# Kernel tuning notes

Hardware: AMD Instinct MI355X
Metric: run time of the kernel (lower is better)

The kernel has to match this reference:

```python
import jax, jax.numpy as jnp
import numpy as np

N_NODES = 100000
N_EDGES = 3200000
IN_F, HID, OUT = 3, 32, 1
NEG_SLOPE = 0.2


def _glorot(key, shape):
    fan_in, fan_out = shape[0], shape[-1]
    lim = jnp.sqrt(6.0 / (fan_in + fan_out)).astype(jnp.float32)
    return jax.random.uniform(key, shape, jnp.float32, -lim, lim)


def setup_inputs() -> dict:
    key = jax.random.key(0)
    ks = jax.random.split(key, 12)
    x = jax.random.normal(ks[0], (N_NODES, IN_F), jnp.float32)
    edge_index = jax.random.randint(ks[1], (2, N_EDGES), 0, N_NODES, jnp.int32)
    return {
        "x": x,
        "edge_index": edge_index,
        "W1": _glorot(ks[2], (IN_F, HID)),
        "att_src1": _glorot(ks[3], (1, HID))[0],
        "att_dst1": _glorot(ks[4], (1, HID))[0],
        "b1": jnp.zeros((HID,), jnp.float32),
        "W2": _glorot(ks[5], (HID, HID)),
        "att_src2": _glorot(ks[6], (1, HID))[0],
        "att_dst2": _glorot(ks[7], (1, HID))[0],
        "b2": jnp.zeros((HID,), jnp.float32),
        "Wl": _glorot(ks[8], (HID, OUT)),
        "bl": jnp.zeros((OUT,), jnp.float32),
    }


def gat_layer(x, src, dst, W, att_src, att_dst, b):
    # h: [N, HID] dense transform
    h = x @ W
    # per-node attention halves (compute once per node, gather per edge)
    a_s = h @ att_src  # [N]
    a_d = h @ att_dst  # [N]
    logits = jax.nn.leaky_relu(a_s[src] + a_d[dst], NEG_SLOPE)  # [E+N]
    # segment-softmax over incoming edges of each dst node
    m = jax.ops.segment_max(logits, dst, num_segments=N_NODES)
    m = jnp.where(jnp.isfinite(m), m, 0.0)
    ex = jnp.exp(logits - m[dst])
    denom = jax.ops.segment_sum(ex, dst, num_segments=N_NODES)
    coef = ex / (denom[dst] + 1e-16)
    # weighted scatter-aggregate of source messages
    out = jax.ops.segment_sum(coef[:, None] * h[src], dst, num_segments=N_NODES)
    return out + b


def reference(x, edge_index, W1, att_src1, att_dst1, b1, W2, att_src2, att_dst2, b2, Wl, bl):
    # PyG GATConv default: add self-loops
    loops = jnp.arange(N_NODES, dtype=edge_index.dtype)
    src = jnp.concatenate([edge_index[0], loops])
    dst = jnp.concatenate([edge_index[1], loops])
    h = gat_layer(x, src, dst, W1, att_src1, att_dst1, b1)
    h = jax.nn.relu(h)  # dropout is identity in eval
    h = gat_layer(h, src, dst, W2, att_src2, att_dst2, b2)
    h = jax.nn.relu(h)
    return h @ Wl + bl
```

## Files before the change

kernel.cpp:

```cpp
#include <hip/hip_runtime.h>
#include <hip/hip_fp16.h>

#define HID 32
#define BN 132
#define NBPAD 1024
#define BSTRIDE 5120
#define CHUNK 8192

__device__ __forceinline__ float lrelu(float x) { return x > 0.0f ? x : 0.2f * x; }

__global__ void k_transform1(const float* __restrict__ x,
                             const float* __restrict__ W1,
                             const float* __restrict__ att_src,
                             const float* __restrict__ att_dst,
                             __half* __restrict__ hh,
                             float* __restrict__ a_s,
                             float* __restrict__ a_d,
                             int* __restrict__ cursor,
                             int N)
{
    int tid = blockIdx.x * blockDim.x + threadIdx.x;
    if (tid < NBPAD) cursor[tid] = 0;
    int n = tid >> 5;
    int f = tid & 31;
    if (n >= N) return;
    float x0 = x[n * 3 + 0], x1 = x[n * 3 + 1], x2 = x[n * 3 + 2];
    float hv = x0 * W1[f] + x1 * W1[HID + f] + x2 * W1[2 * HID + f];
    hh[(size_t)n * HID + f] = __float2half(hv);
    float as = hv * att_src[f];
    float ad = hv * att_dst[f];
    #pragma unroll
    for (int m = 16; m >= 1; m >>= 1) {
        as += __shfl_xor(as, m, 32);
        ad += __shfl_xor(ad, m, 32);
    }
    if (f == 0) { a_s[n] = as; a_d[n] = ad; }
}

__global__ void __launch_bounds__(256) k_binscatter(const int* __restrict__ src,
                                                    const int* __restrict__ dst,
                                                    int* __restrict__ cursor,
                                                    unsigned int* __restrict__ packed,
                                                    int NB, int E)
{
    __shared__ int stage[CHUNK];
    __shared__ int lhist[NBPAD], lexcl[NBPAD], lbase[NBPAD], lcur[NBPAD];
    __shared__ int arr[256];
    int t = threadIdx.x;
    for (int i = t; i < NBPAD; i += 256) { lhist[i] = 0; lcur[i] = 0; }
    __syncthreads();
    int base = blockIdx.x * CHUNK;
    int cnt = E - base; if (cnt > CHUNK) cnt = CHUNK;
    for (int i = t; i < cnt; i += 256)
        atomicAdd(&lhist[dst[base + i] / BN], 1);
    __syncthreads();
    int b0 = 4 * t;
    int c0 = lhist[b0], c1 = lhist[b0 + 1], c2 = lhist[b0 + 2], c3 = lhist[b0 + 3];
    int s = c0 + c1 + c2 + c3;
    arr[t] = s;
    __syncthreads();
    for (int o = 1; o < 256; o <<= 1) {
        int v = (t >= o) ? arr[t - o] : 0;
        __syncthreads();
        arr[t] += v;
        __syncthreads();
    }
    int ex = arr[t] - s;
    lexcl[b0] = ex; lexcl[b0 + 1] = ex + c0;
    lexcl[b0 + 2] = ex + c0 + c1; lexcl[b0 + 3] = ex + c0 + c1 + c2;
    for (int b = t; b < NB; b += 256)
        if (lhist[b]) lbase[b] = b * BSTRIDE + atomicAdd(&cursor[b], lhist[b]);
    __syncthreads();
    for (int i = t; i < cnt; i += 256) {
        int d = dst[base + i];
        int sv = src[base + i];
        int b = d / BN;
        int dl = d - b * BN;
        int idx = lexcl[b] + atomicAdd(&lcur[b], 1);
        stage[idx] = (int)((unsigned)sv | ((unsigned)dl << 17));
    }
    __syncthreads();
    for (int i = t; i < cnt; i += 256) {
        int lo = 0, hi = NB - 1;
        while (lo < hi) {
            int mid = (lo + hi + 1) >> 1;
            if (lexcl[mid] <= i) lo = mid; else hi = mid - 1;
        }
        int gpos = lbase[lo] + (i - lexcl[lo]);
        if (gpos < (lo + 1) * BSTRIDE)
            packed[gpos] = (unsigned)stage[i];
    }
}

__global__ void __launch_bounds__(256) k_bucket_csr(unsigned int* __restrict__ packed,
                                                    const int* __restrict__ cursor,
                                                    int* __restrict__ offsets,
                                                    int* __restrict__ deg, int N)
{
    __shared__ int lcsr[BSTRIDE];
    __shared__ int lhist[256], lscan[256], lcur[256];
    int b = blockIdx.x, t = threadIdx.x;
    int base = b * BSTRIDE;
    int cnt = cursor[b]; if (cnt > BSTRIDE) cnt = BSTRIDE;
    lhist[t] = 0; lcur[t] = 0;
    __syncthreads();
    for (int i = t; i < cnt; i += 256)
        atomicAdd(&lhist[(packed[base + i] >> 17) & 255], 1);
    __syncthreads();
    lscan[t] = lhist[t];
    __syncthreads();
    for (int o = 1; o < 256; o <<= 1) {
        int v = (t >= o) ? lscan[t - o] : 0;
        __syncthreads();
        lscan[t] += v;
        __syncthreads();
    }
    int node = b * BN + t;
    int excl = lscan[t] - lhist[t];
    if (t < BN && node < N) { offsets[node] = base + excl; deg[node] = lhist[t]; }
    for (int i = t; i < cnt; i += 256) {
        unsigned int p = packed[base + i];
        int dl = (p >> 17) & 255;
        int pos = atomicAdd(&lcur[dl], 1);
        lcsr[(lscan[dl] - lhist[dl]) + pos] = (int)(p & 0x1FFFF);
    }
    __syncthreads();
    for (int i = t; i < cnt; i += 256)
        packed[base + i] = (unsigned)lcsr[i];
}

__device__ __forceinline__ void agg_core(const __half* __restrict__ hh,
                                         const float* __restrict__ a_s,
                                         float a_dn, float a_sn,
                                         const float* __restrict__ b,
                                         int n, int f, int off, int dg,
                                         const int* __restrict__ csr_src,
                                         float& vx, float& vy)
{
    float ex = __expf(lrelu(a_sn + a_dn));
    float den = ex;
    float2 hs = __half22float2(*(const __half2*)(hh + (size_t)n * HID + 2 * f));
    float accx = ex * hs.x;
    float accy = ex * hs.y;
    for (int base = 0; base < dg; base += 16) {
        int m = dg - base; if (m > 16) m = 16;
        int sv = 0;
        float exv = 0.0f;
        if (f < m) {
            sv = csr_src[off + base + f];
            exv = __expf(lrelu(a_s[sv] + a_dn));
        }
        int j = 0;
        for (; j + 8 <= m; j += 8) {
            int s0 = __shfl(sv, j, 16), s1 = __shfl(sv, j + 1, 16);
            int s2 = __shfl(sv, j + 2, 16), s3 = __shfl(sv, j + 3, 16);
            int s4 = __shfl(sv, j + 4, 16), s5 = __shfl(sv, j + 5, 16);
            int s6 = __shfl(sv, j + 6, 16), s7 = __shfl(sv, j + 7, 16);
            float e0 = __shfl(exv, j, 16), e1 = __shfl(exv, j + 1, 16);
            float e2 = __shfl(exv, j + 2, 16), e3 = __shfl(exv, j + 3, 16);
            float e4 = __shfl(exv, j + 4, 16), e5 = __shfl(exv, j + 5, 16);
            float e6 = __shfl(exv, j + 6, 16), e7 = __shfl(exv, j + 7, 16);
            __half2 p0 = *(const __half2*)(hh + (size_t)s0 * HID + 2 * f);
            __half2 p1 = *(const __half2*)(hh + (size_t)s1 * HID + 2 * f);
            __half2 p2 = *(const __half2*)(hh + (size_t)s2 * HID + 2 * f);
            __half2 p3 = *(const __half2*)(hh + (size_t)s3 * HID + 2 * f);
            __half2 p4 = *(const __half2*)(hh + (size_t)s4 * HID + 2 * f);
            __half2 p5 = *(const __half2*)(hh + (size_t)s5 * HID + 2 * f);
            __half2 p6 = *(const __half2*)(hh + (size_t)s6 * HID + 2 * f);
            __half2 p7 = *(const __half2*)(hh + (size_t)s7 * HID + 2 * f);
            float2 q0 = __half22float2(p0), q1 = __half22float2(p1);
            float2 q2 = __half22float2(p2), q3 = __half22float2(p3);
            float2 q4 = __half22float2(p4), q5 = __half22float2(p5);
            float2 q6 = __half22float2(p6), q7 = __half22float2(p7);
            den += ((e0 + e1) + (e2 + e3)) + ((e4 + e5) + (e6 + e7));
            accx = fmaf(e0, q0.x, accx); accy = fmaf(e0, q0.y, accy);
            accx = fmaf(e1, q1.x, accx); accy = fmaf(e1, q1.y, accy);
            accx = fmaf(e2, q2.x, accx); accy = fmaf(e2, q2.y, accy);
            accx = fmaf(e3, q3.x, accx); accy = fmaf(e3, q3.y, accy);
            accx = fmaf(e4, q4.x, accx); accy = fmaf(e4, q4.y, accy);
            accx = fmaf(e5, q5.x, accx); accy = fmaf(e5, q5.y, accy);
            accx = fmaf(e6, q6.x, accx); accy = fmaf(e6, q6.y, accy);
            accx = fmaf(e7, q7.x, accx); accy = fmaf(e7, q7.y, accy);
        }
        for (; j + 4 <= m; j += 4) {
            int s0 = __shfl(sv, j, 16), s1 = __shfl(sv, j + 1, 16);
            int s2 = __shfl(sv, j + 2, 16), s3 = __shfl(sv, j + 3, 16);
            float e0 = __shfl(exv, j, 16), e1 = __shfl(exv, j + 1, 16);
            float e2 = __shfl(exv, j + 2, 16), e3 = __shfl(exv, j + 3, 16);
            __half2 p0 = *(const __half2*)(hh + (size_t)s0 * HID + 2 * f);
            __half2 p1 = *(const __half2*)(hh + (size_t)s1 * HID + 2 * f);
            __half2 p2 = *(const __half2*)(hh + (size_t)s2 * HID + 2 * f);
            __half2 p3 = *(const __half2*)(hh + (size_t)s3 * HID + 2 * f);
            float2 q0 = __half22float2(p0), q1 = __half22float2(p1);
            float2 q2 = __half22float2(p2), q3 = __half22float2(p3);
            den += (e0 + e1) + (e2 + e3);
            accx = fmaf(e0, q0.x, accx); accy = fmaf(e0, q0.y, accy);
            accx = fmaf(e1, q1.x, accx); accy = fmaf(e1, q1.y, accy);
            accx = fmaf(e2, q2.x, accx); accy = fmaf(e2, q2.y, accy);
            accx = fmaf(e3, q3.x, accx); accy = fmaf(e3, q3.y, accy);
        }
        for (; j < m; ++j) {
            int s0 = __shfl(sv, j, 16);
            float e0 = __shfl(exv, j, 16);
            float2 q0 = __half22float2(*(const __half2*)(hh + (size_t)s0 * HID + 2 * f));
            den += e0;
            accx = fmaf(e0, q0.x, accx);
            accy = fmaf(e0, q0.y, accy);
        }
    }
    float inv = 1.0f / (den + 1e-16f);
    vx = fmaxf(accx * inv + b[2 * f], 0.0f);
    vy = fmaxf(accy * inv + b[2 * f + 1], 0.0f);
}

__global__ void __launch_bounds__(256) k_agg_mid(const __half* __restrict__ hh,
                          const float* __restrict__ a_s,
                          const float* __restrict__ a_d,
                          const int* __restrict__ offsets,
                          const int* __restrict__ deg,
                          const int* __restrict__ csr_src,
                          const float* __restrict__ b,
                          const float* __restrict__ W2,
                          const float* __restrict__ att_src2,
                          const float* __restrict__ att_dst2,
                          __half* __restrict__ hh_out,
                          float* __restrict__ a_s_out,
                          float* __restrict__ a_d_out,
                          int N)
{
    int tid = blockIdx.x * blockDim.x + threadIdx.x;
    int n = tid >> 4;
    int f = tid & 15;
    if (n >= N) return;
    float vx, vy;
    agg_core(hh, a_s, a_d[n], a_s[n], b, n, f, offsets[n], deg[n], csr_src, vx, vy);
    float hx = 0.0f, hy = 0.0f;
    #pragma unroll
    for (int k = 0; k < 16; ++k) {
        float va = __shfl(vx, k, 16);
        float vb = __shfl(vy, k, 16);
        float2 w0 = *(const float2*)(W2 + (2 * k) * HID + 2 * f);
        float2 w1 = *(const float2*)(W2 + (2 * k + 1) * HID + 2 * f);
        hx = fmaf(va, w0.x, hx); hy = fmaf(va, w0.y, hy);
        hx = fmaf(vb, w1.x, hx); hy = fmaf(vb, w1.y, hy);
    }
    *(__half2*)(hh_out + (size_t)n * HID + 2 * f) = __floats2half2_rn(hx, hy);
    float as = hx * att_src2[2 * f] + hy * att_src2[2 * f + 1];
    float ad = hx * att_dst2[2 * f] + hy * att_dst2[2 * f + 1];
    #pragma unroll
    for (int m2 = 8; m2 >= 1; m2 >>= 1) {
        as += __shfl_xor(as, m2, 16);
        ad += __shfl_xor(ad, m2, 16);
    }
    if (f == 0) { a_s_out[n] = as; a_d_out[n] = ad; }
}

__global__ void __launch_bounds__(256) k_agg_out(const __half* __restrict__ hh,
                          const float* __restrict__ a_s,
                          const float* __restrict__ a_d,
                          const int* __restrict__ offsets,
                          const int* __restrict__ deg,
                          const int* __restrict__ csr_src,
                          const float* __restrict__ b,
                          const float* __restrict__ Wl,
                          const float* __restrict__ bl,
                          float* __restrict__ out,
                          int N)
{
    int tid = blockIdx.x * blockDim.x + threadIdx.x;
    int n = tid >> 4;
    int f = tid & 15;
    if (n >= N) return;
    float vx, vy;
    agg_core(hh, a_s, a_d[n], a_s[n], b, n, f, offsets[n], deg[n], csr_src, vx, vy);
    float y = vx * Wl[2 * f] + vy * Wl[2 * f + 1];
    #pragma unroll
    for (int m2 = 8; m2 >= 1; m2 >>= 1) {
        y += __shfl_xor(y, m2, 16);
    }
    if (f == 0) out[n] = y + bl[0];
}

extern "C" void kernel_launch(void* const* d_in, const int* in_sizes, int n_in,
                              void* d_out, int out_size, void* d_ws, size_t ws_size,
                              hipStream_t stream)
{
    const float* x        = (const float*)d_in[0];
    const int*   eidx     = (const int*)d_in[1];
    const float* W1       = (const float*)d_in[2];
    const float* att_src1 = (const float*)d_in[3];
    const float* att_dst1 = (const float*)d_in[4];
    const float* b1       = (const float*)d_in[5];
    const float* W2       = (const float*)d_in[6];
    const float* att_src2 = (const float*)d_in[7];
    const float* att_dst2 = (const float*)d_in[8];
    const float* b2       = (const float*)d_in[9];
    const float* Wl       = (const float*)d_in[10];
    const float* bl       = (const float*)d_in[11];
    float* out = (float*)d_out;

    int N = in_sizes[0] / 3;
    int E = in_sizes[1] / 2;
    const int* src = eidx;
    const int* dst = eidx + E;
    int NB = (N + BN - 1) / BN;

    size_t szNHh = (size_t)N * HID * 2;
    size_t szN4  = (size_t)N * 4;
    size_t szPK  = (size_t)NB * BSTRIDE * 4;

    char* ws = (char*)d_ws;
    __half* h1h    = (__half*)ws; ws += szNHh;
    __half* h2h    = (__half*)ws; ws += szNHh;
    unsigned int* packed = (unsigned int*)ws; ws += szPK;
    float*  a_s1   = (float*)ws;  ws += szN4;
    float*  a_d1   = (float*)ws;  ws += szN4;
    float*  a_s2   = (float*)ws;  ws += szN4;
    float*  a_d2   = (float*)ws;  ws += szN4;
    int*    deg    = (int*)ws;    ws += szN4;
    int*    offsets= (int*)ws;    ws += szN4;
    int*    cursor = (int*)ws;    ws += NBPAD * 4;

    const int B = 256;
    int gridNode32 = (N * HID + B - 1) / B;
    int gridNode16 = (N * 16 + B - 1) / B;
    int gridBin    = (E + CHUNK - 1) / CHUNK;

    k_transform1<<<gridNode32, B, 0, stream>>>(x, W1, att_src1, att_dst1,
                                               h1h, a_s1, a_d1, cursor, N);
    k_binscatter<<<gridBin, B, 0, stream>>>(src, dst, cursor, packed, NB, E);
    k_bucket_csr<<<NB, B, 0, stream>>>(packed, cursor, offsets, deg, N);
    k_agg_mid<<<gridNode16, B, 0, stream>>>(h1h, a_s1, a_d1, offsets, deg, (const int*)packed,
                                            b1, W2, att_src2, att_dst2,
                                            h2h, a_s2, a_d2, N);
    k_agg_out<<<gridNode16, B, 0, stream>>>(h2h, a_s2, a_d2, offsets, deg, (const int*)packed,
                                            b2, Wl, bl, out, N);
}
```

Before: 272.4 us.

## Fuse bucket CSR build into aggregation kernels and replace binary search with bin-id table

Removes the separate bucket-to-CSR kernel. Each aggregation kernel now rebuilds the per-bucket CSR in shared memory and aggregates that bucket's nodes with 512-thread blocks, one block per bucket. Binscatter drops its per-element binary search for a shared-memory table of bin ids, and CHUNK and NBPAD shrink to 4096 and 768. The intent is to cut one kernel launch and the global CSR round trip, and to avoid keeping offsets and degrees in global memory. In exchange the CSR is built twice and aggregation parallelism drops to about 758 blocks with uneven per-node work.

New measurement: 259.7 us. -4.7%, faster.

```diff
diff --git a/kernel.cpp b/kernel.cpp
--- a/kernel.cpp
+++ b/kernel.cpp
@@ -3,9 +3,9 @@
 
 #define HID 32
 #define BN 132
-#define NBPAD 1024
+#define NBPAD 768
 #define BSTRIDE 5120
-#define CHUNK 8192
+#define CHUNK 4096
 
 __device__ __forceinline__ float lrelu(float x) { return x > 0.0f ? x : 0.2f * x; }
 
@@ -41,9 +41,10 @@
                                                     const int* __restrict__ dst,
                                                     int* __restrict__ cursor,
                                                     unsigned int* __restrict__ packed,
-                                                    int NB, int E)
+                                                    int NBr, int E)
 {
     __shared__ int stage[CHUNK];
+    __shared__ unsigned short sbid[CHUNK];
     __shared__ int lhist[NBPAD], lexcl[NBPAD], lbase[NBPAD], lcur[NBPAD];
     __shared__ int arr[256];
     int t = threadIdx.x;
@@ -54,9 +55,9 @@
     for (int i = t; i < cnt; i += 256)
         atomicAdd(&lhist[dst[base + i] / BN], 1);
     __syncthreads();
-    int b0 = 4 * t;
-    int c0 = lhist[b0], c1 = lhist[b0 + 1], c2 = lhist[b0 + 2], c3 = lhist[b0 + 3];
-    int s = c0 + c1 + c2 + c3;
+    int b0 = 3 * t;
+    int c0 = lhist[b0], c1 = lhist[b0 + 1], c2 = lhist[b0 + 2];
+    int s = c0 + c1 + c2;
     arr[t] = s;
     __syncthreads();
     for (int o = 1; o < 256; o <<= 1) {
@@ -66,9 +67,12 @@
         __syncthreads();
     }
     int ex = arr[t] - s;
-    lexcl[b0] = ex; lexcl[b0 + 1] = ex + c0;
-    lexcl[b0 + 2] = ex + c0 + c1; lexcl[b0 + 3] = ex + c0 + c1 + c2;
-    for (int b = t; b < NB; b += 256)
+    int e0 = ex, e1 = ex + c0, e2 = ex + c0 + c1;
+    lexcl[b0] = e0; lexcl[b0 + 1] = e1; lexcl[b0 + 2] = e2;
+    for (int i = 0; i < c0; ++i) sbid[e0 + i] = (unsigned short)b0;
+    for (int i = 0; i < c1; ++i) sbid[e1 + i] = (unsigned short)(b0 + 1);
+    for (int i = 0; i < c2; ++i) sbid[e2 + i] = (unsigned short)(b0 + 2);
+    for (int b = t; b < NBr; b += 256)
         if (lhist[b]) lbase[b] = b * BSTRIDE + atomicAdd(&cursor[b], lhist[b]);
     __syncthreads();
     for (int i = t; i < cnt; i += 256) {
@@ -81,60 +85,19 @@
     }
     __syncthreads();
     for (int i = t; i < cnt; i += 256) {
-        int lo = 0, hi = NB - 1;
-        while (lo < hi) {
-            int mid = (lo + hi + 1) >> 1;
-            if (lexcl[mid] <= i) lo = mid; else hi = mid - 1;
-        }
-        int gpos = lbase[lo] + (i - lexcl[lo]);
-        if (gpos < (lo + 1) * BSTRIDE)
+        int b = sbid[i];
+        int gpos = lbase[b] + (i - lexcl[b]);
+        if (gpos < (b + 1) * BSTRIDE)
             packed[gpos] = (unsigned)stage[i];
     }
 }
 
-__global__ void __launch_bounds__(256) k_bucket_csr(unsigned int* __restrict__ packed,
-                                                    const int* __restrict__ cursor,
-                                                    int* __restrict__ offsets,
-                                                    int* __restrict__ deg, int N)
-{
-    __shared__ int lcsr[BSTRIDE];
-    __shared__ int lhist[256], lscan[256], lcur[256];
-    int b = blockIdx.x, t = threadIdx.x;
-    int base = b * BSTRIDE;
-    int cnt = cursor[b]; if (cnt > BSTRIDE) cnt = BSTRIDE;
-    lhist[t] = 0; lcur[t] = 0;
-    __syncthreads();
-    for (int i = t; i < cnt; i += 256)
-        atomicAdd(&lhist[(packed[base + i] >> 17) & 255], 1);
-    __syncthreads();
-    lscan[t] = lhist[t];
-    __syncthreads();
-    for (int o = 1; o < 256; o <<= 1) {
-        int v = (t >= o) ? lscan[t - o] : 0;
-        __syncthreads();
-        lscan[t] += v;
-        __syncthreads();
-    }
-    int node = b * BN + t;
-    int excl = lscan[t] - lhist[t];
-    if (t < BN && node < N) { offsets[node] = base + excl; deg[node] = lhist[t]; }
-    for (int i = t; i < cnt; i += 256) {
-        unsigned int p = packed[base + i];
-        int dl = (p >> 17) & 255;
-        int pos = atomicAdd(&lcur[dl], 1);
-        lcsr[(lscan[dl] - lhist[dl]) + pos] = (int)(p & 0x1FFFF);
-    }
-    __syncthreads();
-    for (int i = t; i < cnt; i += 256)
-        packed[base + i] = (unsigned)lcsr[i];
-}
-
-__device__ __forceinline__ void agg_core(const __half* __restrict__ hh,
+__device__ __forceinline__ void agg_node(const __half* __restrict__ hh,
                                          const float* __restrict__ a_s,
                                          float a_dn, float a_sn,
                                          const float* __restrict__ b,
-                                         int n, int f, int off, int dg,
-                                         const int* __restrict__ csr_src,
+                                         int n, int f,
+                                         const int* lcsr, int off, int dg,
                                          float& vx, float& vy)
 {
     float ex = __expf(lrelu(a_sn + a_dn));
@@ -147,7 +110,7 @@
         int sv = 0;
         float exv = 0.0f;
         if (f < m) {
-            sv = csr_src[off + base + f];
+            sv = lcsr[off + base + f];
             exv = __expf(lrelu(a_s[sv] + a_dn));
         }
         int j = 0;
@@ -213,72 +176,112 @@
     vy = fmaxf(accy * inv + b[2 * f + 1], 0.0f);
 }
 
-__global__ void __launch_bounds__(256) k_agg_mid(const __half* __restrict__ hh,
+__device__ __forceinline__ int build_lcsr(const unsigned int* pk, int cnt,
+                                          int* lcsr, int* lhist, int* lscan, int* lcur)
+{
+    int t = threadIdx.x;
+    if (t < 256) { lhist[t] = 0; lcur[t] = 0; }
+    __syncthreads();
+    for (int i = t; i < cnt; i += 512)
+        atomicAdd(&lhist[(pk[i] >> 17) & 255], 1);
+    __syncthreads();
+    if (t < 256) lscan[t] = lhist[t];
+    __syncthreads();
+    for (int o = 1; o < 256; o <<= 1) {
+        int v = (t < 256 && t >= o) ? lscan[t - o] : 0;
+        __syncthreads();
+        if (t < 256) lscan[t] += v;
+        __syncthreads();
+    }
+    for (int i = t; i < cnt; i += 512) {
+        unsigned int p = pk[i];
+        int dl = (p >> 17) & 255;
+        int pos = atomicAdd(&lcur[dl], 1);
+        lcsr[(lscan[dl] - lhist[dl]) + pos] = (int)(p & 0x1FFFF);
+    }
+    __syncthreads();
+    return cnt;
+}
+
+__global__ void __launch_bounds__(512) k_agg_mid_f(const __half* __restrict__ hh,
                           const float* __restrict__ a_s,
                           const float* __restrict__ a_d,
-                          const int* __restrict__ offsets,
-                          const int* __restrict__ deg,
-                          const int* __restrict__ csr_src,
-                          const float* __restrict__ b,
+                          const int* __restrict__ cursor,
+                          const unsigned int* __restrict__ packed,
+                          const float* __restrict__ b1,
                           const float* __restrict__ W2,
-                          const float* __restrict__ att_src2,
-                          const float* __restrict__ att_dst2,
+                          const float* __restrict__ as2w,
+                          const float* __restrict__ ad2w,
                           __half* __restrict__ hh_out,
-                          float* __restrict__ a_s_out,
-                          float* __restrict__ a_d_out,
+                          float* __restrict__ as_out,
+                          float* __restrict__ ad_out,
                           int N)
 {
-    int tid = blockIdx.x * blockDim.x + threadIdx.x;
-    int n = tid >> 4;
-    int f = tid & 15;
-    if (n >= N) return;
-    float vx, vy;
-    agg_core(hh, a_s, a_d[n], a_s[n], b, n, f, offsets[n], deg[n], csr_src, vx, vy);
-    float hx = 0.0f, hy = 0.0f;
-    #pragma unroll
-    for (int k = 0; k < 16; ++k) {
-        float va = __shfl(vx, k, 16);
-        float vb = __shfl(vy, k, 16);
-        float2 w0 = *(const float2*)(W2 + (2 * k) * HID + 2 * f);
-        float2 w1 = *(const float2*)(W2 + (2 * k + 1) * HID + 2 * f);
-        hx = fmaf(va, w0.x, hx); hy = fmaf(va, w0.y, hy);
-        hx = fmaf(vb, w1.x, hx); hy = fmaf(vb, w1.y, hy);
-    }
-    *(__half2*)(hh_out + (size_t)n * HID + 2 * f) = __floats2half2_rn(hx, hy);
-    float as = hx * att_src2[2 * f] + hy * att_src2[2 * f + 1];
-    float ad = hx * att_dst2[2 * f] + hy * att_dst2[2 * f + 1];
-    #pragma unroll
-    for (int m2 = 8; m2 >= 1; m2 >>= 1) {
-        as += __shfl_xor(as, m2, 16);
-        ad += __shfl_xor(ad, m2, 16);
-    }
-    if (f == 0) { a_s_out[n] = as; a_d_out[n] = ad; }
-}
-
-__global__ void __launch_bounds__(256) k_agg_out(const __half* __restrict__ hh,
+    __shared__ int lcsr[BSTRIDE];
+    __shared__ int lhist[256], lscan[256], lcur[256];
+    int bk = blockIdx.x, t = threadIdx.x;
+    int cnt = cursor[bk]; if (cnt > BSTRIDE) cnt = BSTRIDE;
+    build_lcsr(packed + (size_t)bk * BSTRIDE, cnt, lcsr, lhist, lscan, lcur);
+    int g = t >> 4, f = t & 15;
+    for (int dl = g; dl < BN; dl += 32) {
+        int n = bk * BN + dl;
+        if (n >= N) continue;
+        int off = lscan[dl] - lhist[dl];
+        int dg = lhist[dl];
+        float vx, vy;
+        agg_node(hh, a_s, a_d[n], a_s[n], b1, n, f, lcsr, off, dg, vx, vy);
+        float hx = 0.0f, hy = 0.0f;
+        #pragma unroll
+        for (int k = 0; k < 16; ++k) {
+            float va = __shfl(vx, k, 16);
+            float vb = __shfl(vy, k, 16);
+            float2 w0 = *(const float2*)(W2 + (2 * k) * HID + 2 * f);
+            float2 w1 = *(const float2*)(W2 + (2 * k + 1) * HID + 2 * f);
+            hx = fmaf(va, w0.x, hx); hy = fmaf(va, w0.y, hy);
+            hx = fmaf(vb, w1.x, hx); hy = fmaf(vb, w1.y, hy);
+        }
+        *(__half2*)(hh_out + (size_t)n * HID + 2 * f) = __floats2half2_rn(hx, hy);
+        float as = hx * as2w[2 * f] + hy * as2w[2 * f + 1];
+        float ad = hx * ad2w[2 * f] + hy * ad2w[2 * f + 1];
+        #pragma unroll
+        for (int m2 = 8; m2 >= 1; m2 >>= 1) {
+            as += __shfl_xor(as, m2, 16);
+            ad += __shfl_xor(ad, m2, 16);
+        }
+        if (f == 0) { as_out[n] = as; ad_out[n] = ad; }
+    }
+}
+
+__global__ void __launch_bounds__(512) k_agg_out_f(const __half* __restrict__ hh,
                           const float* __restrict__ a_s,
                           const float* __restrict__ a_d,
-                          const int* __restrict__ offsets,
-                          const int* __restrict__ deg,
-                          const int* __restrict__ csr_src,
-                          const float* __restrict__ b,
+                          const int* __restrict__ cursor,
+                          const unsigned int* __restrict__ packed,
+                          const float* __restrict__ b2,
                           const float* __restrict__ Wl,
                           const float* __restrict__ bl,
                           float* __restrict__ out,
                           int N)
 {
-    int tid = blockIdx.x * blockDim.x + threadIdx.x;
-    int n = tid >> 4;
-    int f = tid & 15;
-    if (n >= N) return;
-    float vx, vy;
-    agg_core(hh, a_s, a_d[n], a_s[n], b, n, f, offsets[n], deg[n], csr_src, vx, vy);
-    float y = vx * Wl[2 * f] + vy * Wl[2 * f + 1];
-    #pragma unroll
-    for (int m2 = 8; m2 >= 1; m2 >>= 1) {
-        y += __shfl_xor(y, m2, 16);
-    }
-    if (f == 0) out[n] = y + bl[0];
+    __shared__ int lcsr[BSTRIDE];
+    __shared__ int lhist[256], lscan[256], lcur[256];
+    int bk = blockIdx.x, t = threadIdx.x;
+    int cnt = cursor[bk]; if (cnt > BSTRIDE) cnt = BSTRIDE;
+    build_lcsr(packed + (size_t)bk * BSTRIDE, cnt, lcsr, lhist, lscan, lcur);
+    int g = t >> 4, f = t & 15;
+    for (int dl = g; dl < BN; dl += 32) {
+        int n = bk * BN + dl;
+        if (n >= N) continue;
+        int off = lscan[dl] - lhist[dl];
+        int dg = lhist[dl];
+        float vx, vy;
+        agg_node(hh, a_s, a_d[n], a_s[n], b2, n, f, lcsr, off, dg, vx, vy);
+        float y = vx * Wl[2 * f] + vy * Wl[2 * f + 1];
+        #pragma unroll
+        for (int m2 = 8; m2 >= 1; m2 >>= 1)
+            y += __shfl_xor(y, m2, 16);
+        if (f == 0) out[n] = y + bl[0];
+    }
 }
 
 extern "C" void kernel_launch(void* const* d_in, const int* in_sizes, int n_in,
@@ -303,11 +306,11 @@
     int E = in_sizes[1] / 2;
     const int* src = eidx;
     const int* dst = eidx + E;
-    int NB = (N + BN - 1) / BN;
+    int NBr = (N + BN - 1) / BN;
 
     size_t szNHh = (size_t)N * HID * 2;
     size_t szN4  = (size_t)N * 4;
-    size_t szPK  = (size_t)NB * BSTRIDE * 4;
+    size_t szPK  = (size_t)NBr * BSTRIDE * 4;
 
     char* ws = (char*)d_ws;
     __half* h1h    = (__half*)ws; ws += szNHh;
@@ -317,22 +320,18 @@
     float*  a_d1   = (float*)ws;  ws += szN4;
     float*  a_s2   = (float*)ws;  ws += szN4;
     float*  a_d2   = (float*)ws;  ws += szN4;
-    int*    deg    = (int*)ws;    ws += szN4;
-    int*    offsets= (int*)ws;    ws += szN4;
     int*    cursor = (int*)ws;    ws += NBPAD * 4;
 
     const int B = 256;
     int gridNode32 = (N * HID + B - 1) / B;
-    int gridNode16 = (N * 16 + B - 1) / B;
     int gridBin    = (E + CHUNK - 1) / CHUNK;
 
     k_transform1<<<gridNode32, B, 0, stream>>>(x, W1, att_src1, att_dst1,
                                                h1h, a_s1, a_d1, cursor, N);
-    k_binscatter<<<gridBin, B, 0, stream>>>(src, dst, cursor, packed, NB, E);
-    k_bucket_csr<<<NB, B, 0, stream>>>(packed, cursor, offsets, deg, N);
-    k_agg_mid<<<gridNode16, B, 0, stream>>>(h1h, a_s1, a_d1, offsets, deg, (const int*)packed,
-                                            b1, W2, att_src2, att_dst2,
-                                            h2h, a_s2, a_d2, N);
-    k_agg_out<<<gridNode16, B, 0, stream>>>(h2h, a_s2, a_d2, offsets, deg, (const int*)packed,
-                                            b2, Wl, bl, out, N);
-}
+    k_binscatter<<<gridBin, B, 0, stream>>>(src, dst, cursor, packed, NBr, E);
+    k_agg_mid_f<<<NBr, 512, 0, stream>>>(h1h, a_s1, a_d1, cursor, packed,
+                                         b1, W2, att_src2, att_dst2,
+                                         h2h, a_s2, a_d2, N);
+    k_agg_out_f<<<NBr, 512, 0, stream>>>(h2h, a_s2, a_d2, cursor, packed,
+                                         b2, Wl, bl, out, N);
+}
```
